# Kernel tuning notes

Hardware: AMD Instinct MI355X
Metric: run time of the kernel (lower is better)

Reference implementation:

```python
import jax, jax.numpy as jnp
import numpy as np

N = 16384       # reservoir units (square)
B = 512         # flattened batch rows
NNZ = 131072    # non-zeros in sparse reservoir (avg degree 8)
R = 3           # recurrence_degree -> R+1 steps


def setup_inputs() -> dict:
    key = jax.random.key(0)
    k1, k2, k3, k4, k5, k6, k7 = jax.random.split(key, 7)
    x = jax.random.normal(k1, (B, N), dtype=jnp.float32)
    # sparse reservoir values, scaled for stable recurrence
    kernel = jax.random.normal(k2, (NNZ,), dtype=jnp.float32) * 0.05
    b_i = jax.random.normal(k3, (N,), dtype=jnp.float32) * 0.1
    b_f = jax.random.normal(k4, (N,), dtype=jnp.float32) * 0.1
    b_o = jax.random.normal(k5, (N,), dtype=jnp.float32) * 0.1
    b_g = jax.random.normal(k6, (N,), dtype=jnp.float32) * 0.1
    sparse_indices = jax.random.randint(k7, (NNZ, 2), 0, N, dtype=jnp.int64)
    return {"x": x, "kernel": kernel, "b_i": b_i, "b_f": b_f,
            "b_o": b_o, "b_g": b_g, "sparse_indices": sparse_indices}


def _spmm(h, rows, cols, vals):
    # y = h @ W_sparse, W in COO: y[:, c] += h[:, r] * v
    contrib = h.T[rows] * vals[:, None]              # (nnz, B)
    return jax.ops.segment_sum(contrib, cols, num_segments=N).T  # (B, N)


def reference(x, kernel, b_i, b_f, b_o, b_g, sparse_indices):
    rows = sparse_indices[:, 0]
    cols = sparse_indices[:, 1]
    h = x
    c = jnp.zeros_like(x)
    for _ in range(R + 1):
        z = _spmm(h, rows, cols, kernel)             # shared sparse reservoir matmul
        i = jax.nn.sigmoid(z + b_i)
        f = jax.nn.sigmoid(z + b_f)
        o = jax.nn.sigmoid(z + b_o)
        g = jnp.tanh(z + b_g)
        c = f * c + i * g
        h = o * jnp.tanh(c)
    return h
```

## Files before the change

kernel.cpp:

```cpp
#include <hip/hip_runtime.h>
#include <hip/hip_fp16.h>

#define N 16384
#define B 512
#define NNZ 131072
#define KMAX 16

__device__ __forceinline__ float rcp_(float x) {
    return __builtin_amdgcn_rcpf(x);
}
__device__ __forceinline__ float tanh_(float x) {
    return 1.f - 2.f * rcp_(__expf(2.f * x) + 1.f);
}
__device__ __forceinline__ __half2 as_h2(unsigned int u) {
    __half2 h;
    __builtin_memcpy(&h, &u, 4);
    return h;
}
__device__ __forceinline__ unsigned int pack_h2(float a, float b) {
    __half2 h = __halves2half2(__float2half_rn(a), __float2half_rn(b));
    unsigned int u;
    __builtin_memcpy(&u, &h, 4);
    return u;
}

__device__ __forceinline__ int is64_(const int* __restrict__ w) {
    int a = 1;
    #pragma unroll
    for (int i = 1; i < 16; i += 2) a &= (w[i] == 0);
    return a;
}

__global__ void fill_ell_kernel(const int* __restrict__ w, const float* __restrict__ kern,
                                int* __restrict__ counts, unsigned int* __restrict__ ell,
                                uint2* __restrict__ ovf, int* __restrict__ ovf_cnt) {
    int k = blockIdx.x * 256 + threadIdx.x;
    int is64 = is64_(w);
    int row = is64 ? w[4 * k]     : w[2 * k];
    int col = is64 ? w[4 * k + 2] : w[2 * k + 1];
    unsigned int packed = (unsigned int)(unsigned short)row |
                          ((unsigned int)__half_as_ushort(__float2half_rn(kern[k])) << 16);
    int slot = atomicAdd(&counts[col], 1);
    if (slot < KMAX) {
        ell[col * KMAX + slot] = packed;
    } else {
        int pos = atomicAdd(ovf_cnt, 1);
        ovf[pos] = make_uint2((unsigned int)col, packed);
    }
}

__global__ void pack_bias_kernel(const float* __restrict__ bi, const float* __restrict__ bf,
                                 const float* __restrict__ bo, const float* __restrict__ bg,
                                 float4* __restrict__ b4) {
    int i = blockIdx.x * 256 + threadIdx.x;
    b4[i] = make_float4(__expf(-bi[i]), __expf(-bf[i]), __expf(-bo[i]),
                        __expf(-2.f * bg[i]));
}

__global__ void transpose_f32_f16_kernel(const float* __restrict__ in, __half* __restrict__ out,
                                         int rows, int cols) {
    __shared__ float tile[32][33];
    int bx = blockIdx.x * 32, by = blockIdx.y * 32;
    int tx = threadIdx.x, ty = threadIdx.y;
    for (int i = 0; i < 32; i += 8)
        tile[ty + i][tx] = in[(size_t)(by + ty + i) * cols + (bx + tx)];
    __syncthreads();
    for (int i = 0; i < 32; i += 8)
        out[(size_t)(bx + ty + i) * rows + (by + tx)] = __float2half(tile[tx][ty + i]);
}

template <bool FIRST, bool LAST>
__global__ __launch_bounds__(256) void lstm_iter_kernel(
        const uint2*  __restrict__ hin,
        uint2*        __restrict__ hout,
        uint2*        __restrict__ c,
        float*        __restrict__ out,
        const int*    __restrict__ counts,
        const uint4*  __restrict__ ell4,
        const uint2*  __restrict__ ovf,
        const int*    __restrict__ ovf_cnt,
        const float4* __restrict__ b4) {
    const int t      = threadIdx.x;
    const int lane16 = t & 15;
    const int sub    = t >> 4;
    const int q      = blockIdx.x & 7;
    const int col    = (blockIdx.x >> 3) * 16 + sub;
    const int boff   = q * 16 + lane16;

    uint4 e0 = ell4[col * 4 + 0];
    uint4 e1 = ell4[col * 4 + 1];
    uint4 e2 = ell4[col * 4 + 2];
    uint4 e3 = ell4[col * 4 + 3];
    unsigned int en[KMAX] = { e0.x, e0.y, e0.z, e0.w, e1.x, e1.y, e1.z, e1.w,
                              e2.x, e2.y, e2.z, e2.w, e3.x, e3.y, e3.z, e3.w };

    uint2 hv[KMAX];
    #pragma unroll
    for (int j = 0; j < KMAX; ++j)
        hv[j] = hin[(en[j] & 0xFFFFu) * (B / 4) + boff];

    float z[4] = {0.f, 0.f, 0.f, 0.f};
    #pragma unroll
    for (int j = 0; j < KMAX; ++j) {
        float v = __half2float(__ushort_as_half((unsigned short)(en[j] >> 16)));
        float2 fa = __half22float2(as_h2(hv[j].x));
        float2 fb = __half22float2(as_h2(hv[j].y));
        z[0] = fmaf(v, fa.x, z[0]);
        z[1] = fmaf(v, fa.y, z[1]);
        z[2] = fmaf(v, fb.x, z[2]);
        z[3] = fmaf(v, fb.y, z[3]);
    }
    int cnt = counts[col];
    if (cnt > KMAX) {
        int novf = *ovf_cnt;
        for (int k = 0; k < novf; ++k) {
            uint2 o = ovf[k];
            if (o.x == (unsigned int)col) {
                unsigned int p = o.y;
                float v = __half2float(__ushort_as_half((unsigned short)(p >> 16)));
                uint2 hx = hin[(p & 0xFFFFu) * (B / 4) + boff];
                float2 fa = __half22float2(as_h2(hx.x));
                float2 fb = __half22float2(as_h2(hx.y));
                z[0] = fmaf(v, fa.x, z[0]);
                z[1] = fmaf(v, fa.y, z[1]);
                z[2] = fmaf(v, fb.x, z[2]);
                z[3] = fmaf(v, fb.y, z[3]);
            }
        }
    }

    const float4 bb = b4[col];
    const unsigned int idx = (unsigned int)col * (B / 4) + boff;

    float cv[4] = {0.f, 0.f, 0.f, 0.f};
    if (!FIRST) {
        uint2 cr = c[idx];
        float2 ca = __half22float2(as_h2(cr.x));
        float2 cb = __half22float2(as_h2(cr.y));
        cv[0] = ca.x; cv[1] = ca.y; cv[2] = cb.x; cv[3] = cb.y;
    }

    float hh[4], ch[4];
    #pragma unroll
    for (int e = 0; e < 4; ++e) {
        float ez = __expf(-z[e]);
        float ig = rcp_(fmaf(bb.x, ez, 1.f));
        float fg = rcp_(fmaf(bb.y, ez, 1.f));
        float og = rcp_(fmaf(bb.z, ez, 1.f));
        float dE = bb.w * ez * ez;
        float gg = fmaf(2.f, rcp_(1.f + dE), -1.f);
        float cn = fg * cv[e] + ig * gg;
        ch[e] = cn;
        hh[e] = og * tanh_(cn);
    }

    if (!LAST) {
        c[idx]    = make_uint2(pack_h2(ch[0], ch[1]), pack_h2(ch[2], ch[3]));
        hout[idx] = make_uint2(pack_h2(hh[0], hh[1]), pack_h2(hh[2], hh[3]));
    } else {
        __shared__ float tile[64 * 17];
        #pragma unroll
        for (int e = 0; e < 4; ++e)
            tile[(lane16 * 4 + e) * 17 + sub] = hh[e];
        __syncthreads();
        const int col0 = (blockIdx.x >> 3) * 16;
        #pragma unroll
        for (int k = 0; k < 4; ++k) {
            int i = k * 256 + t;
            int r = i >> 4;
            int cc = i & 15;
            out[(size_t)(q * 64 + r) * N + col0 + cc] = tile[r * 17 + cc];
        }
    }
}

extern "C" void kernel_launch(void* const* d_in, const int* in_sizes, int n_in,
                              void* d_out, int out_size, void* d_ws, size_t ws_size,
                              hipStream_t stream) {
    const float* x    = (const float*)d_in[0];
    const float* kern = (const float*)d_in[1];
    const float* b_i  = (const float*)d_in[2];
    const float* b_f  = (const float*)d_in[3];
    const float* b_o  = (const float*)d_in[4];
    const float* b_g  = (const float*)d_in[5];
    const int*   idxw = (const int*)d_in[6];

    char* ws = (char*)d_ws;
    uint2*        hA      = (uint2*)       (ws + 0);
    uint2*        hB      = (uint2*)       (ws + 16777216);
    uint2*        c       = (uint2*)       (ws + 33554432);
    unsigned int* ell     = (unsigned int*)(ws + 50331648);
    int*          counts  = (int*)         (ws + 51380224);
    int*          ovf_cnt = (int*)         (ws + 51445760);
    uint2*        ovf     = (uint2*)       (ws + 51445768);
    float4*       b4      = (float4*)      (ws + 51478536 + 120);

    hipMemsetAsync(ell, 0, 1048576 + 65536 + 4, stream);

    fill_ell_kernel<<<NNZ / 256, 256, 0, stream>>>(idxw, kern, counts, ell, ovf, ovf_cnt);
    pack_bias_kernel<<<N / 256, 256, 0, stream>>>(b_i, b_f, b_o, b_g, b4);

    transpose_f32_f16_kernel<<<dim3(N / 32, B / 32), dim3(32, 8), 0, stream>>>(
        x, (__half*)hA, B, N);

    const uint4* ell4 = (const uint4*)ell;
    float* out = (float*)d_out;
    const int GRID = (N / 16) * 8;

    lstm_iter_kernel<true,  false><<<GRID, 256, 0, stream>>>(hA, hB, c, out, counts, ell4, ovf, ovf_cnt, b4);
    lstm_iter_kernel<false, false><<<GRID, 256, 0, stream>>>(hB, hA, c, out, counts, ell4, ovf, ovf_cnt, b4);
    lstm_iter_kernel<false, false><<<GRID, 256, 0, stream>>>(hA, hB, c, out, counts, ell4, ovf, ovf_cnt, b4);
    lstm_iter_kernel<false, true ><<<GRID, 256, 0, stream>>>(hB, hA, c, out, counts, ell4, ovf, ovf_cnt, b4);
}
```

Baseline: 226.8 us.

## Widen LSTM threads to 8 batch elements and fuse prep kernels

Each thread in the LSTM step kernel now handles 8 fp16 batch values through 16-byte loads instead of 4 through 8-byte loads. This halves the grid and amortizes the ELL index loads and decode over twice the work. The gathers are split into two batches of 8 and a launch bound of 4 blocks is added to contain register pressure. The transpose, ELL fill and bias pack kernels are merged into one launch to cut launch overhead, at the cost of fewer threads in flight for latency hiding.

```diff
diff --git a/kernel.cpp b/kernel.cpp
--- a/kernel.cpp
+++ b/kernel.cpp
@@ -31,49 +31,54 @@
     return a;
 }
 
-__global__ void fill_ell_kernel(const int* __restrict__ w, const float* __restrict__ kern,
-                                int* __restrict__ counts, unsigned int* __restrict__ ell,
-                                uint2* __restrict__ ovf, int* __restrict__ ovf_cnt) {
-    int k = blockIdx.x * 256 + threadIdx.x;
-    int is64 = is64_(w);
-    int row = is64 ? w[4 * k]     : w[2 * k];
-    int col = is64 ? w[4 * k + 2] : w[2 * k + 1];
-    unsigned int packed = (unsigned int)(unsigned short)row |
-                          ((unsigned int)__half_as_ushort(__float2half_rn(kern[k])) << 16);
-    int slot = atomicAdd(&counts[col], 1);
-    if (slot < KMAX) {
-        ell[col * KMAX + slot] = packed;
+__global__ __launch_bounds__(256) void prep_kernel(
+        const float* __restrict__ x, __half* __restrict__ xT,
+        const int* __restrict__ w, const float* __restrict__ kern,
+        int* __restrict__ counts, unsigned int* __restrict__ ell,
+        uint2* __restrict__ ovf, int* __restrict__ ovf_cnt,
+        const float* __restrict__ bi, const float* __restrict__ bf,
+        const float* __restrict__ bo, const float* __restrict__ bg,
+        float4* __restrict__ b4) {
+    const int bid = blockIdx.x;
+    const int t = threadIdx.x;
+    if (bid < 8192) {
+        __shared__ float tile[32][33];
+        int bx = (bid & 511) * 32;
+        int by = (bid >> 9) * 32;
+        int tx = t & 31, ty = t >> 5;
+        #pragma unroll
+        for (int i = 0; i < 32; i += 8)
+            tile[ty + i][tx] = x[(size_t)(by + ty + i) * N + bx + tx];
+        __syncthreads();
+        #pragma unroll
+        for (int i = 0; i < 32; i += 8)
+            xT[(size_t)(bx + ty + i) * B + by + tx] = __float2half(tile[tx][ty + i]);
+    } else if (bid < 8704) {
+        int k = (bid - 8192) * 256 + t;
+        int is64 = is64_(w);
+        int row = is64 ? w[4 * k]     : w[2 * k];
+        int col = is64 ? w[4 * k + 2] : w[2 * k + 1];
+        unsigned int packed = (unsigned int)(unsigned short)row |
+                              ((unsigned int)__half_as_ushort(__float2half_rn(kern[k])) << 16);
+        int slot = atomicAdd(&counts[col], 1);
+        if (slot < KMAX) {
+            ell[col * KMAX + slot] = packed;
+        } else {
+            int pos = atomicAdd(ovf_cnt, 1);
+            ovf[pos] = make_uint2((unsigned int)col, packed);
+        }
     } else {
-        int pos = atomicAdd(ovf_cnt, 1);
-        ovf[pos] = make_uint2((unsigned int)col, packed);
-    }
-}
-
-__global__ void pack_bias_kernel(const float* __restrict__ bi, const float* __restrict__ bf,
-                                 const float* __restrict__ bo, const float* __restrict__ bg,
-                                 float4* __restrict__ b4) {
-    int i = blockIdx.x * 256 + threadIdx.x;
-    b4[i] = make_float4(__expf(-bi[i]), __expf(-bf[i]), __expf(-bo[i]),
-                        __expf(-2.f * bg[i]));
-}
-
-__global__ void transpose_f32_f16_kernel(const float* __restrict__ in, __half* __restrict__ out,
-                                         int rows, int cols) {
-    __shared__ float tile[32][33];
-    int bx = blockIdx.x * 32, by = blockIdx.y * 32;
-    int tx = threadIdx.x, ty = threadIdx.y;
-    for (int i = 0; i < 32; i += 8)
-        tile[ty + i][tx] = in[(size_t)(by + ty + i) * cols + (bx + tx)];
-    __syncthreads();
-    for (int i = 0; i < 32; i += 8)
-        out[(size_t)(bx + ty + i) * rows + (by + tx)] = __float2half(tile[tx][ty + i]);
+        int i = (bid - 8704) * 256 + t;
+        b4[i] = make_float4(__expf(-bi[i]), __expf(-bf[i]), __expf(-bo[i]),
+                            __expf(-2.f * bg[i]));
+    }
 }
 
 template <bool FIRST, bool LAST>
-__global__ __launch_bounds__(256) void lstm_iter_kernel(
-        const uint2*  __restrict__ hin,
-        uint2*        __restrict__ hout,
-        uint2*        __restrict__ c,
+__global__ __launch_bounds__(256, 4) void lstm_iter_kernel(
+        const uint4*  __restrict__ hin,
+        uint4*        __restrict__ hout,
+        uint4*        __restrict__ c,
         float*        __restrict__ out,
         const int*    __restrict__ counts,
         const uint4*  __restrict__ ell4,
@@ -83,8 +88,8 @@
     const int t      = threadIdx.x;
     const int lane16 = t & 15;
     const int sub    = t >> 4;
-    const int q      = blockIdx.x & 7;
-    const int col    = (blockIdx.x >> 3) * 16 + sub;
+    const int q      = blockIdx.x & 3;
+    const int col    = (blockIdx.x >> 2) * 16 + sub;
     const int boff   = q * 16 + lane16;
 
     uint4 e0 = ell4[col * 4 + 0];
@@ -94,21 +99,25 @@
     unsigned int en[KMAX] = { e0.x, e0.y, e0.z, e0.w, e1.x, e1.y, e1.z, e1.w,
                               e2.x, e2.y, e2.z, e2.w, e3.x, e3.y, e3.z, e3.w };
 
-    uint2 hv[KMAX];
+    float z[8] = {0.f, 0.f, 0.f, 0.f, 0.f, 0.f, 0.f, 0.f};
     #pragma unroll
-    for (int j = 0; j < KMAX; ++j)
-        hv[j] = hin[(en[j] & 0xFFFFu) * (B / 4) + boff];
-
-    float z[4] = {0.f, 0.f, 0.f, 0.f};
-    #pragma unroll
-    for (int j = 0; j < KMAX; ++j) {
-        float v = __half2float(__ushort_as_half((unsigned short)(en[j] >> 16)));
-        float2 fa = __half22float2(as_h2(hv[j].x));
-        float2 fb = __half22float2(as_h2(hv[j].y));
-        z[0] = fmaf(v, fa.x, z[0]);
-        z[1] = fmaf(v, fa.y, z[1]);
-        z[2] = fmaf(v, fb.x, z[2]);
-        z[3] = fmaf(v, fb.y, z[3]);
+    for (int half = 0; half < 2; ++half) {
+        uint4 hv[8];
+        #pragma unroll
+        for (int j = 0; j < 8; ++j)
+            hv[j] = hin[(en[half * 8 + j] & 0xFFFFu) * (B / 8) + boff];
+        #pragma unroll
+        for (int j = 0; j < 8; ++j) {
+            float v = __half2float(__ushort_as_half((unsigned short)(en[half * 8 + j] >> 16)));
+            float2 f0 = __half22float2(as_h2(hv[j].x));
+            float2 f1 = __half22float2(as_h2(hv[j].y));
+            float2 f2 = __half22float2(as_h2(hv[j].z));
+            float2 f3 = __half22float2(as_h2(hv[j].w));
+            z[0] = fmaf(v, f0.x, z[0]);  z[1] = fmaf(v, f0.y, z[1]);
+            z[2] = fmaf(v, f1.x, z[2]);  z[3] = fmaf(v, f1.y, z[3]);
+            z[4] = fmaf(v, f2.x, z[4]);  z[5] = fmaf(v, f2.y, z[5]);
+            z[6] = fmaf(v, f3.x, z[6]);  z[7] = fmaf(v, f3.y, z[7]);
+        }
     }
     int cnt = counts[col];
     if (cnt > KMAX) {
@@ -118,31 +127,36 @@
             if (o.x == (unsigned int)col) {
                 unsigned int p = o.y;
                 float v = __half2float(__ushort_as_half((unsigned short)(p >> 16)));
-                uint2 hx = hin[(p & 0xFFFFu) * (B / 4) + boff];
-                float2 fa = __half22float2(as_h2(hx.x));
-                float2 fb = __half22float2(as_h2(hx.y));
-                z[0] = fmaf(v, fa.x, z[0]);
-                z[1] = fmaf(v, fa.y, z[1]);
-                z[2] = fmaf(v, fb.x, z[2]);
-                z[3] = fmaf(v, fb.y, z[3]);
+                uint4 hx = hin[(p & 0xFFFFu) * (B / 8) + boff];
+                float2 f0 = __half22float2(as_h2(hx.x));
+                float2 f1 = __half22float2(as_h2(hx.y));
+                float2 f2 = __half22float2(as_h2(hx.z));
+                float2 f3 = __half22float2(as_h2(hx.w));
+                z[0] = fmaf(v, f0.x, z[0]);  z[1] = fmaf(v, f0.y, z[1]);
+                z[2] = fmaf(v, f1.x, z[2]);  z[3] = fmaf(v, f1.y, z[3]);
+                z[4] = fmaf(v, f2.x, z[4]);  z[5] = fmaf(v, f2.y, z[5]);
+                z[6] = fmaf(v, f3.x, z[6]);  z[7] = fmaf(v, f3.y, z[7]);
             }
         }
     }
 
     const float4 bb = b4[col];
-    const unsigned int idx = (unsigned int)col * (B / 4) + boff;
-
-    float cv[4] = {0.f, 0.f, 0.f, 0.f};
+    const unsigned int idx = (unsigned int)col * (B / 8) + boff;
+
+    float cv[8] = {0.f, 0.f, 0.f, 0.f, 0.f, 0.f, 0.f, 0.f};
     if (!FIRST) {
-        uint2 cr = c[idx];
-        float2 ca = __half22float2(as_h2(cr.x));
-        float2 cb = __half22float2(as_h2(cr.y));
-        cv[0] = ca.x; cv[1] = ca.y; cv[2] = cb.x; cv[3] = cb.y;
-    }
-
-    float hh[4], ch[4];
+        uint4 cr = c[idx];
+        float2 c0 = __half22float2(as_h2(cr.x));
+        float2 c1 = __half22float2(as_h2(cr.y));
+        float2 c2 = __half22float2(as_h2(cr.z));
+        float2 c3 = __half22float2(as_h2(cr.w));
+        cv[0] = c0.x; cv[1] = c0.y; cv[2] = c1.x; cv[3] = c1.y;
+        cv[4] = c2.x; cv[5] = c2.y; cv[6] = c3.x; cv[7] = c3.y;
+    }
+
+    float hh[8], ch[8];
     #pragma unroll
-    for (int e = 0; e < 4; ++e) {
+    for (int e = 0; e < 8; ++e) {
         float ez = __expf(-z[e]);
         float ig = rcp_(fmaf(bb.x, ez, 1.f));
         float fg = rcp_(fmaf(bb.y, ez, 1.f));
@@ -155,21 +169,23 @@
     }
 
     if (!LAST) {
-        c[idx]    = make_uint2(pack_h2(ch[0], ch[1]), pack_h2(ch[2], ch[3]));
-        hout[idx] = make_uint2(pack_h2(hh[0], hh[1]), pack_h2(hh[2], hh[3]));
+        c[idx]    = make_uint4(pack_h2(ch[0], ch[1]), pack_h2(ch[2], ch[3]),
+                               pack_h2(ch[4], ch[5]), pack_h2(ch[6], ch[7]));
+        hout[idx] = make_uint4(pack_h2(hh[0], hh[1]), pack_h2(hh[2], hh[3]),
+                               pack_h2(hh[4], hh[5]), pack_h2(hh[6], hh[7]));
     } else {
-        __shared__ float tile[64 * 17];
-        #pragma unroll
-        for (int e = 0; e < 4; ++e)
-            tile[(lane16 * 4 + e) * 17 + sub] = hh[e];
+        __shared__ float tile[128 * 17];
+        #pragma unroll
+        for (int e = 0; e < 8; ++e)
+            tile[(lane16 * 8 + e) * 17 + sub] = hh[e];
         __syncthreads();
-        const int col0 = (blockIdx.x >> 3) * 16;
-        #pragma unroll
-        for (int k = 0; k < 4; ++k) {
+        const int col0 = (blockIdx.x >> 2) * 16;
+        #pragma unroll
+        for (int k = 0; k < 8; ++k) {
             int i = k * 256 + t;
             int r = i >> 4;
             int cc = i & 15;
-            out[(size_t)(q * 64 + r) * N + col0 + cc] = tile[r * 17 + cc];
+            out[(size_t)(q * 128 + r) * N + col0 + cc] = tile[r * 17 + cc];
         }
     }
 }
@@ -186,26 +202,24 @@
     const int*   idxw = (const int*)d_in[6];
 
     char* ws = (char*)d_ws;
-    uint2*        hA      = (uint2*)       (ws + 0);
-    uint2*        hB      = (uint2*)       (ws + 16777216);
-    uint2*        c       = (uint2*)       (ws + 33554432);
+    uint4*        hA      = (uint4*)       (ws + 0);
+    uint4*        hB      = (uint4*)       (ws + 16777216);
+    uint4*        c       = (uint4*)       (ws + 33554432);
     unsigned int* ell     = (unsigned int*)(ws + 50331648);
     int*          counts  = (int*)         (ws + 51380224);
     int*          ovf_cnt = (int*)         (ws + 51445760);
     uint2*        ovf     = (uint2*)       (ws + 51445768);
-    float4*       b4      = (float4*)      (ws + 51478536 + 120);
+    float4*       b4      = (float4*)      (ws + 51478656);
 
     hipMemsetAsync(ell, 0, 1048576 + 65536 + 4, stream);
 
-    fill_ell_kernel<<<NNZ / 256, 256, 0, stream>>>(idxw, kern, counts, ell, ovf, ovf_cnt);
-    pack_bias_kernel<<<N / 256, 256, 0, stream>>>(b_i, b_f, b_o, b_g, b4);
-
-    transpose_f32_f16_kernel<<<dim3(N / 32, B / 32), dim3(32, 8), 0, stream>>>(
-        x, (__half*)hA, B, N);
+    prep_kernel<<<8768, 256, 0, stream>>>(x, (__half*)hA, idxw, kern,
+                                          counts, ell, ovf, ovf_cnt,
+                                          b_i, b_f, b_o, b_g, b4);
 
     const uint4* ell4 = (const uint4*)ell;
     float* out = (float*)d_out;
-    const int GRID = (N / 16) * 8;
+    const int GRID = (N / 16) * 4;
 
     lstm_iter_kernel<true,  false><<<GRID, 256, 0, stream>>>(hA, hB, c, out, counts, ell4, ovf, ovf_cnt, b4);
     lstm_iter_kernel<false, false><<<GRID, 256, 0, stream>>>(hB, hA, c, out, counts, ell4, ovf, ovf_cnt, b4);
```

Result: faster. 208.8 us (-7.9%).
